# Kernel optimization log

Hardware: AMD Instinct MI355X
Metric: run time of the kernel (lower is better)

## Reference

```python
import jax, jax.numpy as jnp
import numpy as np

D_IN = 768
D_H = 256
N_CTX = 4

def setup_inputs() -> dict:
    key = jax.random.key(0)
    ks = jax.random.split(key, 6)
    b, s = 64, 2048
    return {
        "last_hidden_states": jax.random.normal(ks[0], (b, s, D_IN), dtype=jnp.float32),
        "W1": jax.random.normal(ks[1], (D_IN, D_H), dtype=jnp.float32) / np.sqrt(D_IN),
        "b1": jnp.zeros((D_H,), dtype=jnp.float32),
        "context_vector": jax.random.normal(ks[2], (D_H, N_CTX), dtype=jnp.float32),
        "W2": jax.random.normal(ks[3], (N_CTX * D_IN, D_IN), dtype=jnp.float32) / np.sqrt(N_CTX * D_IN),
        "b2": jnp.zeros((D_IN,), dtype=jnp.float32),
    }

def reference(last_hidden_states, W1, b1, context_vector, W2, b2):
    b = last_hidden_states.shape[0]
    # h: [b, s, 256]
    h = jnp.tanh(jnp.einsum('bsd,dh->bsh', last_hidden_states, W1) + b1)
    # scores over sequence dim for each of 4 context vectors: [b, s, 4]
    scores = jax.nn.softmax(jnp.einsum('bsh,hc->bsc', h, context_vector), axis=1)
    # weighted sums: [b, 4, 768] -> flatten to [b, 3072]
    pooled = jnp.einsum('bsc,bsd->bcd', scores, last_hidden_states).reshape(b, -1)
    pooled = jax.nn.relu(pooled)
    return pooled @ W2 + b2
```

## Files before the change

### kernel.cpp

```cpp
#include <hip/hip_runtime.h>

typedef _Float16 f16x8 __attribute__((ext_vector_type(8)));
typedef float f32x4 __attribute__((ext_vector_type(4)));

#define D_IN 768
#define D_H  256
#define SEQ  2048

__global__ __launch_bounds__(256) void k0_w1t(const float* __restrict__ W1,
                                              _Float16* __restrict__ W1T) {
  __shared__ float tl[64][65];
  const int kb = blockIdx.x, nb = blockIdx.y, t = threadIdx.x;
#pragma unroll
  for (int rep = 0; rep < 16; ++rep) {
    const int row = rep * 4 + (t >> 6), col = t & 63;
    tl[row][col] = W1[(size_t)(kb * 64 + row) * D_H + nb * 64 + col];
  }
  __syncthreads();
#pragma unroll
  for (int rep = 0; rep < 16; ++rep) {
    const int n = rep * 4 + (t >> 6), k = t & 63;
    W1T[(size_t)(nb * 64 + n) * D_IN + kb * 64 + k] = (_Float16)tl[k][n];
  }
}

__global__ __launch_bounds__(512, 2) void kf_fused(const float* __restrict__ X,
    const _Float16* __restrict__ W1T, const float* __restrict__ b1,
    const float* __restrict__ C, _Float16* __restrict__ Ppart,
    float* __restrict__ stats) {
  __shared__ _Float16 Xl[32][776];
  __shared__ float red2[8][32][4];
  __shared__ float red[32][4];
  const int t = threadIdx.x;
  const int bid = blockIdx.x;
  const size_t M0 = (size_t)bid * 32;

  const int xr = t >> 4, xk = (t & 15) * 8;
  const float* Ag = X + (M0 + xr) * D_IN + xk;
  float4 a[12];
#pragma unroll
  for (int s = 0; s < 6; ++s) {
    a[2 * s]     = *(const float4*)(Ag + s * 128);
    a[2 * s + 1] = *(const float4*)(Ag + s * 128 + 4);
  }
#pragma unroll
  for (int s = 0; s < 6; ++s) {
    f16x8 h;
    h[0] = (_Float16)a[2*s].x;   h[1] = (_Float16)a[2*s].y;
    h[2] = (_Float16)a[2*s].z;   h[3] = (_Float16)a[2*s].w;
    h[4] = (_Float16)a[2*s+1].x; h[5] = (_Float16)a[2*s+1].y;
    h[6] = (_Float16)a[2*s+1].z; h[7] = (_Float16)a[2*s+1].w;
    *(f16x8*)&Xl[xr][xk + s * 128] = h;
  }
  __syncthreads();

  const int lane = t & 63, wn = t >> 6;
  const int l15 = lane & 15, kg = lane >> 4;
  const _Float16* Bg0 = W1T + (size_t)(wn * 32 + l15) * D_IN + kg * 8;
  const _Float16* Bg1 = Bg0 + (size_t)16 * D_IN;

  f32x4 acc[2][2];
#pragma unroll
  for (int i = 0; i < 2; ++i)
#pragma unroll
    for (int j = 0; j < 2; ++j) acc[i][j] = f32x4{0.f, 0.f, 0.f, 0.f};

#pragma unroll
  for (int kt = 0; kt < 12; ++kt) {
    f16x8 bf[2][2], af[2][2];
#pragma unroll
    for (int st = 0; st < 2; ++st) {
      bf[0][st] = *(const f16x8*)(Bg0 + kt * 64 + st * 32);
      bf[1][st] = *(const f16x8*)(Bg1 + kt * 64 + st * 32);
      af[0][st] = *(const f16x8*)&Xl[l15][kt * 64 + st * 32 + kg * 8];
      af[1][st] = *(const f16x8*)&Xl[16 + l15][kt * 64 + st * 32 + kg * 8];
    }
#pragma unroll
    for (int st = 0; st < 2; ++st)
#pragma unroll
      for (int j = 0; j < 2; ++j)
#pragma unroll
        for (int i = 0; i < 2; ++i)
          acc[i][j] = __builtin_amdgcn_mfma_f32_16x16x32_f16(af[i][st], bf[j][st], acc[i][j], 0, 0, 0);
  }

  float part[2][4][4];
#pragma unroll
  for (int i = 0; i < 2; ++i)
#pragma unroll
    for (int r = 0; r < 4; ++r)
#pragma unroll
      for (int c = 0; c < 4; ++c) part[i][r][c] = 0.f;

#pragma unroll
  for (int j = 0; j < 2; ++j) {
    const int col = wn * 32 + j * 16 + l15;
    const float4 c4 = *(const float4*)(C + col * 4);
    const float bv = b1[col];
#pragma unroll
    for (int i = 0; i < 2; ++i)
#pragma unroll
      for (int r = 0; r < 4; ++r) {
        float z = acc[i][j][r] + bv;
        z = fminf(fmaxf(z, -15.f), 15.f);
        const float e = __expf(2.f * z);
        const float h = (e - 1.f) / (e + 1.f);
        part[i][r][0] += h * c4.x;
        part[i][r][1] += h * c4.y;
        part[i][r][2] += h * c4.z;
        part[i][r][3] += h * c4.w;
      }
  }
#pragma unroll
  for (int off = 1; off < 16; off <<= 1) {
#pragma unroll
    for (int i = 0; i < 2; ++i)
#pragma unroll
      for (int r = 0; r < 4; ++r)
#pragma unroll
        for (int c = 0; c < 4; ++c)
          part[i][r][c] += __shfl_xor(part[i][r][c], off, 64);
  }
  if (l15 == 0) {
#pragma unroll
    for (int i = 0; i < 2; ++i)
#pragma unroll
      for (int r = 0; r < 4; ++r)
#pragma unroll
        for (int c = 0; c < 4; ++c)
          red2[wn][i * 16 + kg * 4 + r][c] = part[i][r][c];
  }
  __syncthreads();

  if (t < 128) {
    const int r = t >> 2, c = t & 3;
    float v = 0.f;
#pragma unroll
    for (int w = 0; w < 8; ++w) v += red2[w][r][c];
    red[r][c] = v;
  }
  __syncthreads();
  if (t < 256) {
    const int c = t >> 6, r = t & 63;
    const float v = (r < 32) ? red[r][c] : -3.4e38f;
    float m = v;
#pragma unroll
    for (int off = 1; off < 64; off <<= 1) m = fmaxf(m, __shfl_xor(m, off, 64));
    const float e = (r < 32) ? __expf(v - m) : 0.f;
    if (r < 32) red[r][c] = e;
    float s = e;
#pragma unroll
    for (int off = 1; off < 64; off <<= 1) s += __shfl_xor(s, off, 64);
    if (r == 0) {
      stats[(size_t)bid * 8 + c * 2]     = m;
      stats[(size_t)bid * 8 + c * 2 + 1] = s;
    }
  }
  __syncthreads();

  const int pc = t >> 7, pch = t & 127;
  if (pch < 96) {
    float a8[8] = {0.f, 0.f, 0.f, 0.f, 0.f, 0.f, 0.f, 0.f};
#pragma unroll 4
    for (int r = 0; r < 32; ++r) {
      const float w = red[r][pc];
      const f16x8 x8 = *(const f16x8*)&Xl[r][pch * 8];
#pragma unroll
      for (int k = 0; k < 8; ++k) a8[k] += w * (float)x8[k];
    }
    f16x8 o;
#pragma unroll
    for (int k = 0; k < 8; ++k) o[k] = (_Float16)a8[k];
    *(f16x8*)&Ppart[(size_t)bid * 3072 + pc * 768 + pch * 8] = o;
  }
}

__global__ __launch_bounds__(256) void kc_combine(const _Float16* __restrict__ Ppart,
    const float* __restrict__ stats, float* __restrict__ pooled) {
  const int b = blockIdx.x, t = threadIdx.x;
  __shared__ float sm[64][8];
  __shared__ float Mc[4], Dc[4], fw[64][4];
  sm[t >> 2][(t & 3) * 2]     = stats[((size_t)b * 64 + (t >> 2)) * 8 + (t & 3) * 2];
  sm[t >> 2][(t & 3) * 2 + 1] = stats[((size_t)b * 64 + (t >> 2)) * 8 + (t & 3) * 2 + 1];
  __syncthreads();
  if (t < 4) {
    float m = sm[0][t * 2];
#pragma unroll 8
    for (int blk = 1; blk < 64; ++blk) m = fmaxf(m, sm[blk][t * 2]);
    Mc[t] = m;
  }
  __syncthreads();
  {
    const int blk = t >> 2, c = t & 3;
    fw[blk][c] = __expf(sm[blk][c * 2] - Mc[c]);
  }
  __syncthreads();
  if (t < 4) {
    float s = 0.f;
#pragma unroll 8
    for (int blk = 0; blk < 64; ++blk) s += fw[blk][t] * sm[blk][t * 2 + 1];
    Dc[t] = 1.f / s;
  }
  __syncthreads();
#pragma unroll
  for (int c = 0; c < 4; ++c) {
#pragma unroll
    for (int rep = 0; rep < 3; ++rep) {
      const int d = rep * 256 + t;
      float acc = 0.f;
#pragma unroll 8
      for (int blk = 0; blk < 64; ++blk)
        acc += fw[blk][c] * (float)Ppart[((size_t)(b * 64 + blk)) * 3072 + c * 768 + d];
      pooled[(size_t)b * 3072 + c * 768 + d] = fmaxf(acc * Dc[c], 0.f);
    }
  }
}

__global__ __launch_bounds__(256) void k4_partial(const float* __restrict__ pooled,
                                                  const float* __restrict__ W2,
                                                  float* __restrict__ partial) {
  const int jc = blockIdx.x, kc = blockIdx.y, t = threadIdx.x;
  __shared__ float plds[64 * 192];
  __shared__ float sum2[64][64];
  for (int idx = t; idx < 64 * 192; idx += 256) {
    const int b = idx / 192, k = idx - b * 192;
    plds[idx] = pooled[(size_t)b * 3072 + kc * 192 + k];
  }
  __syncthreads();
  const int j = t & 63, kp = t >> 6;
  float acc[64];
#pragma unroll
  for (int b = 0; b < 64; ++b) acc[b] = 0.f;
  const float* W2p = W2 + (size_t)(kc * 192 + kp * 48) * D_IN + jc * 64 + j;
  const float* pb = plds + kp * 48;
  for (int ki = 0; ki < 48; ki += 4) {
    const float w0 = W2p[(size_t)(ki + 0) * D_IN];
    const float w1 = W2p[(size_t)(ki + 1) * D_IN];
    const float w2 = W2p[(size_t)(ki + 2) * D_IN];
    const float w3 = W2p[(size_t)(ki + 3) * D_IN];
#pragma unroll
    for (int b = 0; b < 64; ++b) {
      const float4 p4 = *(const float4*)(pb + b * 192 + ki);
      acc[b] += p4.x * w0 + p4.y * w1 + p4.z * w2 + p4.w * w3;
    }
  }
#pragma unroll
  for (int p = 0; p < 4; ++p) {
    if (kp == p) {
      if (p == 0) {
#pragma unroll
        for (int b = 0; b < 64; ++b) sum2[b][j] = acc[b];
      } else {
#pragma unroll
        for (int b = 0; b < 64; ++b) sum2[b][j] += acc[b];
      }
    }
    __syncthreads();
  }
  for (int idx = t; idx < 4096; idx += 256) {
    const int b = idx >> 6, jj = idx & 63;
    partial[(size_t)kc * 49152 + (size_t)b * D_IN + jc * 64 + jj] = sum2[b][jj];
  }
}

__global__ __launch_bounds__(256) void k5_final(const float* __restrict__ partial,
                                                const float* __restrict__ b2,
                                                float* __restrict__ out) {
  const int o = blockIdx.x * 256 + threadIdx.x;
  float v = b2[o % D_IN];
#pragma unroll
  for (int p = 0; p < 16; ++p) v += partial[(size_t)p * 49152 + o];
  out[o] = v;
}

extern "C" void kernel_launch(void* const* d_in, const int* in_sizes, int n_in,
                              void* d_out, int out_size, void* d_ws, size_t ws_size,
                              hipStream_t stream) {
  const float* X  = (const float*)d_in[0];
  const float* W1 = (const float*)d_in[1];
  const float* b1 = (const float*)d_in[2];
  const float* C  = (const float*)d_in[3];
  const float* W2 = (const float*)d_in[4];
  const float* b2 = (const float*)d_in[5];
  float* out = (float*)d_out;
  char* ws = (char*)d_ws;
  _Float16* W1T   = (_Float16*)ws;
  float* pooled   = (float*)(ws + 393216);
  float* stats    = (float*)(ws + 1179648);
  _Float16* Ppart = (_Float16*)(ws + 1310720);
  float* partial  = (float*)(ws + 1310720);

  k0_w1t    <<<dim3(12, 4), 256, 0, stream>>>(W1, W1T);
  kf_fused  <<<4096,        512, 0, stream>>>(X, W1T, b1, C, Ppart, stats);
  kc_combine<<<64,          256, 0, stream>>>(Ppart, stats, pooled);
  k4_partial<<<dim3(12,16), 256, 0, stream>>>(pooled, W2, partial);
  k5_final  <<<192,         256, 0, stream>>>(partial, b2, out);
}
```

Measured before the change: 324.2 us.

## Restructure fused GEMM to 64-row tiles with async global-to-LDS K-streaming

```diff
diff --git a/kernel.cpp b/kernel.cpp
--- a/kernel.cpp
+++ b/kernel.cpp
@@ -1,11 +1,18 @@
 #include <hip/hip_runtime.h>
 
 typedef _Float16 f16x8 __attribute__((ext_vector_type(8)));
+typedef _Float16 f16x4 __attribute__((ext_vector_type(4)));
 typedef float f32x4 __attribute__((ext_vector_type(4)));
 
 #define D_IN 768
 #define D_H  256
 #define SEQ  2048
+
+__device__ __forceinline__ void gld16(const void* g, void* l) {
+  __builtin_amdgcn_global_load_lds(
+      (const __attribute__((address_space(1))) unsigned int*)g,
+      (__attribute__((address_space(3))) unsigned int*)l, 16, 0, 0);
+}
 
 __global__ __launch_bounds__(256) void k0_w1t(const float* __restrict__ W1,
                                               _Float16* __restrict__ W1T) {
@@ -24,64 +31,83 @@
   }
 }
 
-__global__ __launch_bounds__(512, 2) void kf_fused(const float* __restrict__ X,
+__global__ __launch_bounds__(256, 4) void kf_fused(const float* __restrict__ X,
     const _Float16* __restrict__ W1T, const float* __restrict__ b1,
     const float* __restrict__ C, _Float16* __restrict__ Ppart,
     float* __restrict__ stats) {
-  __shared__ _Float16 Xl[32][776];
-  __shared__ float red2[8][32][4];
-  __shared__ float red[32][4];
+  __shared__ float    Al[64][32];
+  __shared__ _Float16 Bl[256][32];
+  __shared__ float    red2[2][64][4];
+  __shared__ float    red[64][4];
   const int t = threadIdx.x;
   const int bid = blockIdx.x;
-  const size_t M0 = (size_t)bid * 32;
-
-  const int xr = t >> 4, xk = (t & 15) * 8;
-  const float* Ag = X + (M0 + xr) * D_IN + xk;
-  float4 a[12];
-#pragma unroll
-  for (int s = 0; s < 6; ++s) {
-    a[2 * s]     = *(const float4*)(Ag + s * 128);
-    a[2 * s + 1] = *(const float4*)(Ag + s * 128 + 4);
-  }
-#pragma unroll
-  for (int s = 0; s < 6; ++s) {
-    f16x8 h;
-    h[0] = (_Float16)a[2*s].x;   h[1] = (_Float16)a[2*s].y;
-    h[2] = (_Float16)a[2*s].z;   h[3] = (_Float16)a[2*s].w;
-    h[4] = (_Float16)a[2*s+1].x; h[5] = (_Float16)a[2*s+1].y;
-    h[6] = (_Float16)a[2*s+1].z; h[7] = (_Float16)a[2*s+1].w;
-    *(f16x8*)&Xl[xr][xk + s * 128] = h;
-  }
-  __syncthreads();
-
-  const int lane = t & 63, wn = t >> 6;
-  const int l15 = lane & 15, kg = lane >> 4;
-  const _Float16* Bg0 = W1T + (size_t)(wn * 32 + l15) * D_IN + kg * 8;
-  const _Float16* Bg1 = Bg0 + (size_t)16 * D_IN;
-
-  f32x4 acc[2][2];
+  const size_t M0 = (size_t)bid * 64;
+
+  const int l = t & 63, w = t >> 6;
+  const int ar0 = (w * 2 + 0) * 8 + (l >> 3);
+  const int ar1 = (w * 2 + 1) * 8 + (l >> 3);
+  const int aj = l & 7;
+  const float* As0 = X + (M0 + ar0) * D_IN + ((aj ^ (ar0 & 7)) * 4);
+  const float* As1 = X + (M0 + ar1) * D_IN + ((aj ^ (ar1 & 7)) * 4);
+  char* Ad0 = (char*)Al + (w * 2 + 0) * 1024 + l * 16;
+  char* Ad1 = (char*)Al + (w * 2 + 1) * 1024 + l * 16;
+  const int bj = l & 3;
+  const int bc0 = (w * 4 + 0) * 16 + (l >> 2);
+  const int bc1 = (w * 4 + 1) * 16 + (l >> 2);
+  const int bc2 = (w * 4 + 2) * 16 + (l >> 2);
+  const int bc3 = (w * 4 + 3) * 16 + (l >> 2);
+  const _Float16* Bs0 = W1T + (size_t)bc0 * D_IN + ((bj ^ (bc0 & 3)) * 8);
+  const _Float16* Bs1 = W1T + (size_t)bc1 * D_IN + ((bj ^ (bc1 & 3)) * 8);
+  const _Float16* Bs2 = W1T + (size_t)bc2 * D_IN + ((bj ^ (bc2 & 3)) * 8);
+  const _Float16* Bs3 = W1T + (size_t)bc3 * D_IN + ((bj ^ (bc3 & 3)) * 8);
+  char* Bd0 = (char*)Bl + (w * 4 + 0) * 1024 + l * 16;
+  char* Bd1 = (char*)Bl + (w * 4 + 1) * 1024 + l * 16;
+  char* Bd2 = (char*)Bl + (w * 4 + 2) * 1024 + l * 16;
+  char* Bd3 = (char*)Bl + (w * 4 + 3) * 1024 + l * 16;
+
+  const int wm = w >> 1, wn = w & 1;
+  const int l15 = l & 15, kg = l >> 4;
+  const int r0 = wm * 32 + l15, r1 = r0 + 16;
+  const int sA0lo = ((2 * kg) ^ (r0 & 7)) * 4, sA0hi = ((2 * kg + 1) ^ (r0 & 7)) * 4;
+  const int sA1lo = ((2 * kg) ^ (r1 & 7)) * 4, sA1hi = ((2 * kg + 1) ^ (r1 & 7)) * 4;
+
+  f32x4 acc[2][8];
 #pragma unroll
   for (int i = 0; i < 2; ++i)
 #pragma unroll
-    for (int j = 0; j < 2; ++j) acc[i][j] = f32x4{0.f, 0.f, 0.f, 0.f};
-
-#pragma unroll
-  for (int kt = 0; kt < 12; ++kt) {
-    f16x8 bf[2][2], af[2][2];
-#pragma unroll
-    for (int st = 0; st < 2; ++st) {
-      bf[0][st] = *(const f16x8*)(Bg0 + kt * 64 + st * 32);
-      bf[1][st] = *(const f16x8*)(Bg1 + kt * 64 + st * 32);
-      af[0][st] = *(const f16x8*)&Xl[l15][kt * 64 + st * 32 + kg * 8];
-      af[1][st] = *(const f16x8*)&Xl[16 + l15][kt * 64 + st * 32 + kg * 8];
-    }
-#pragma unroll
-    for (int st = 0; st < 2; ++st)
-#pragma unroll
-      for (int j = 0; j < 2; ++j)
-#pragma unroll
-        for (int i = 0; i < 2; ++i)
-          acc[i][j] = __builtin_amdgcn_mfma_f32_16x16x32_f16(af[i][st], bf[j][st], acc[i][j], 0, 0, 0);
+    for (int n = 0; n < 8; ++n) acc[i][n] = f32x4{0.f, 0.f, 0.f, 0.f};
+
+  for (int kt = 0; kt < 24; ++kt) {
+    const int ko = kt * 32;
+    gld16(As0 + ko, Ad0);
+    gld16(As1 + ko, Ad1);
+    gld16(Bs0 + ko, Bd0);
+    gld16(Bs1 + ko, Bd1);
+    gld16(Bs2 + ko, Bd2);
+    gld16(Bs3 + ko, Bd3);
+    __syncthreads();
+
+    const float4 a0lo = *(const float4*)&Al[r0][sA0lo];
+    const float4 a0hi = *(const float4*)&Al[r0][sA0hi];
+    const float4 a1lo = *(const float4*)&Al[r1][sA1lo];
+    const float4 a1hi = *(const float4*)&Al[r1][sA1hi];
+    f16x8 af0, af1;
+    af0[0] = (_Float16)a0lo.x; af0[1] = (_Float16)a0lo.y;
+    af0[2] = (_Float16)a0lo.z; af0[3] = (_Float16)a0lo.w;
+    af0[4] = (_Float16)a0hi.x; af0[5] = (_Float16)a0hi.y;
+    af0[6] = (_Float16)a0hi.z; af0[7] = (_Float16)a0hi.w;
+    af1[0] = (_Float16)a1lo.x; af1[1] = (_Float16)a1lo.y;
+    af1[2] = (_Float16)a1lo.z; af1[3] = (_Float16)a1lo.w;
+    af1[4] = (_Float16)a1hi.x; af1[5] = (_Float16)a1hi.y;
+    af1[6] = (_Float16)a1hi.z; af1[7] = (_Float16)a1hi.w;
+#pragma unroll
+    for (int n = 0; n < 8; ++n) {
+      const int col = wn * 128 + n * 16 + l15;
+      const f16x8 bf = *(const f16x8*)&Bl[col][(kg ^ (col & 3)) * 8];
+      acc[0][n] = __builtin_amdgcn_mfma_f32_16x16x32_f16(af0, bf, acc[0][n], 0, 0, 0);
+      acc[1][n] = __builtin_amdgcn_mfma_f32_16x16x32_f16(af1, bf, acc[1][n], 0, 0, 0);
+    }
+    __syncthreads();
   }
 
   float part[2][4][4];
@@ -93,15 +119,15 @@
       for (int c = 0; c < 4; ++c) part[i][r][c] = 0.f;
 
 #pragma unroll
-  for (int j = 0; j < 2; ++j) {
-    const int col = wn * 32 + j * 16 + l15;
+  for (int n = 0; n < 8; ++n) {
+    const int col = wn * 128 + n * 16 + l15;
     const float4 c4 = *(const float4*)(C + col * 4);
     const float bv = b1[col];
 #pragma unroll
     for (int i = 0; i < 2; ++i)
 #pragma unroll
       for (int r = 0; r < 4; ++r) {
-        float z = acc[i][j][r] + bv;
+        float z = acc[i][n][r] + bv;
         z = fminf(fmaxf(z, -15.f), 15.f);
         const float e = __expf(2.f * z);
         const float h = (e - 1.f) / (e + 1.f);
@@ -128,26 +154,23 @@
       for (int r = 0; r < 4; ++r)
 #pragma unroll
         for (int c = 0; c < 4; ++c)
-          red2[wn][i * 16 + kg * 4 + r][c] = part[i][r][c];
-  }
-  __syncthreads();
-
-  if (t < 128) {
+          red2[wn][wm * 32 + i * 16 + kg * 4 + r][c] = part[i][r][c];
+  }
+  __syncthreads();
+
+  {
     const int r = t >> 2, c = t & 3;
-    float v = 0.f;
-#pragma unroll
-    for (int w = 0; w < 8; ++w) v += red2[w][r][c];
-    red[r][c] = v;
-  }
-  __syncthreads();
-  if (t < 256) {
+    red[r][c] = red2[0][r][c] + red2[1][r][c];
+  }
+  __syncthreads();
+  {
     const int c = t >> 6, r = t & 63;
-    const float v = (r < 32) ? red[r][c] : -3.4e38f;
+    const float v = red[r][c];
     float m = v;
 #pragma unroll
     for (int off = 1; off < 64; off <<= 1) m = fmaxf(m, __shfl_xor(m, off, 64));
-    const float e = (r < 32) ? __expf(v - m) : 0.f;
-    if (r < 32) red[r][c] = e;
+    const float e = __expf(v - m);
+    red[r][c] = e;
     float s = e;
 #pragma unroll
     for (int off = 1; off < 64; off <<= 1) s += __shfl_xor(s, off, 64);
@@ -158,47 +181,57 @@
   }
   __syncthreads();
 
-  const int pc = t >> 7, pch = t & 127;
-  if (pch < 96) {
-    float a8[8] = {0.f, 0.f, 0.f, 0.f, 0.f, 0.f, 0.f, 0.f};
+  if (t < 192) {
+    float pacc[4][4];
+#pragma unroll
+    for (int c = 0; c < 4; ++c)
+#pragma unroll
+      for (int j = 0; j < 4; ++j) pacc[c][j] = 0.f;
+    const float* Xp = X + M0 * D_IN + t * 4;
 #pragma unroll 4
-    for (int r = 0; r < 32; ++r) {
-      const float w = red[r][pc];
-      const f16x8 x8 = *(const f16x8*)&Xl[r][pch * 8];
-#pragma unroll
-      for (int k = 0; k < 8; ++k) a8[k] += w * (float)x8[k];
-    }
-    f16x8 o;
-#pragma unroll
-    for (int k = 0; k < 8; ++k) o[k] = (_Float16)a8[k];
-    *(f16x8*)&Ppart[(size_t)bid * 3072 + pc * 768 + pch * 8] = o;
+    for (int r = 0; r < 64; ++r) {
+      const float4 x4 = *(const float4*)(Xp + (size_t)r * D_IN);
+      const float4 w4 = *(const float4*)&red[r][0];
+      const float wc[4] = {w4.x, w4.y, w4.z, w4.w};
+      const float xv[4] = {x4.x, x4.y, x4.z, x4.w};
+#pragma unroll
+      for (int c = 0; c < 4; ++c)
+#pragma unroll
+        for (int j = 0; j < 4; ++j) pacc[c][j] += wc[c] * xv[j];
+    }
+#pragma unroll
+    for (int c = 0; c < 4; ++c) {
+      f16x4 o;
+#pragma unroll
+      for (int j = 0; j < 4; ++j) o[j] = (_Float16)pacc[c][j];
+      *(f16x4*)&Ppart[(size_t)bid * 3072 + c * 768 + t * 4] = o;
+    }
   }
 }
 
 __global__ __launch_bounds__(256) void kc_combine(const _Float16* __restrict__ Ppart,
     const float* __restrict__ stats, float* __restrict__ pooled) {
   const int b = blockIdx.x, t = threadIdx.x;
-  __shared__ float sm[64][8];
-  __shared__ float Mc[4], Dc[4], fw[64][4];
-  sm[t >> 2][(t & 3) * 2]     = stats[((size_t)b * 64 + (t >> 2)) * 8 + (t & 3) * 2];
-  sm[t >> 2][(t & 3) * 2 + 1] = stats[((size_t)b * 64 + (t >> 2)) * 8 + (t & 3) * 2 + 1];
+  __shared__ float sm[32][8];
+  __shared__ float Mc[4], Dc[4], fw[32][4];
+  sm[t >> 3][t & 7] = stats[((size_t)b * 32 + (t >> 3)) * 8 + (t & 7)];
   __syncthreads();
   if (t < 4) {
     float m = sm[0][t * 2];
-#pragma unroll 8
-    for (int blk = 1; blk < 64; ++blk) m = fmaxf(m, sm[blk][t * 2]);
+#pragma unroll
+    for (int blk = 1; blk < 32; ++blk) m = fmaxf(m, sm[blk][t * 2]);
     Mc[t] = m;
   }
   __syncthreads();
-  {
+  if (t < 128) {
     const int blk = t >> 2, c = t & 3;
     fw[blk][c] = __expf(sm[blk][c * 2] - Mc[c]);
   }
   __syncthreads();
   if (t < 4) {
     float s = 0.f;
-#pragma unroll 8
-    for (int blk = 0; blk < 64; ++blk) s += fw[blk][t] * sm[blk][t * 2 + 1];
+#pragma unroll
+    for (int blk = 0; blk < 32; ++blk) s += fw[blk][t] * sm[blk][t * 2 + 1];
     Dc[t] = 1.f / s;
   }
   __syncthreads();
@@ -208,9 +241,9 @@
     for (int rep = 0; rep < 3; ++rep) {
       const int d = rep * 256 + t;
       float acc = 0.f;
-#pragma unroll 8
-      for (int blk = 0; blk < 64; ++blk)
-        acc += fw[blk][c] * (float)Ppart[((size_t)(b * 64 + blk)) * 3072 + c * 768 + d];
+#pragma unroll 4
+      for (int blk = 0; blk < 32; ++blk)
+        acc += fw[blk][c] * (float)Ppart[((size_t)(b * 32 + blk)) * 3072 + c * 768 + d];
       pooled[(size_t)b * 3072 + c * 768 + d] = fmaxf(acc * Dc[c], 0.f);
     }
   }
@@ -287,11 +320,11 @@
   _Float16* W1T   = (_Float16*)ws;
   float* pooled   = (float*)(ws + 393216);
   float* stats    = (float*)(ws + 1179648);
-  _Float16* Ppart = (_Float16*)(ws + 1310720);
-  float* partial  = (float*)(ws + 1310720);
+  _Float16* Ppart = (_Float16*)(ws + 1245184);
+  float* partial  = (float*)(ws + 1245184);
 
   k0_w1t    <<<dim3(12, 4), 256, 0, stream>>>(W1, W1T);
-  kf_fused  <<<4096,        512, 0, stream>>>(X, W1T, b1, C, Ppart, stats);
+  kf_fused  <<<2048,        256, 0, stream>>>(X, W1T, b1, C, Ppart, stats);
   kc_combine<<<64,          256, 0, stream>>>(Ppart, stats, pooled);
   k4_partial<<<dim3(12,16), 256, 0, stream>>>(pooled, W2, partial);
   k5_final  <<<192,         256, 0, stream>>>(partial, b2, out);
```

Measured after the change: 307.5 us. 5.1% less time.

## Shrink fused block to 256 threads with wider per-wave N tile

Applied to the files above, without the earlier changes.

```diff
diff --git a/kernel.cpp b/kernel.cpp
--- a/kernel.cpp
+++ b/kernel.cpp
@@ -1,6 +1,7 @@
 #include <hip/hip_runtime.h>
 
 typedef _Float16 f16x8 __attribute__((ext_vector_type(8)));
+typedef _Float16 f16x4 __attribute__((ext_vector_type(4)));
 typedef float f32x4 __attribute__((ext_vector_type(4)));
 
 #define D_IN 768
@@ -24,64 +25,67 @@
   }
 }
 
-__global__ __launch_bounds__(512, 2) void kf_fused(const float* __restrict__ X,
+__global__ __launch_bounds__(256, 3) void kf_fused(const float* __restrict__ X,
     const _Float16* __restrict__ W1T, const float* __restrict__ b1,
     const float* __restrict__ C, _Float16* __restrict__ Ppart,
     float* __restrict__ stats) {
   __shared__ _Float16 Xl[32][776];
-  __shared__ float red2[8][32][4];
+  __shared__ float red2[4][32][4];
   __shared__ float red[32][4];
   const int t = threadIdx.x;
   const int bid = blockIdx.x;
   const size_t M0 = (size_t)bid * 32;
 
-  const int xr = t >> 4, xk = (t & 15) * 8;
-  const float* Ag = X + (M0 + xr) * D_IN + xk;
-  float4 a[12];
-#pragma unroll
-  for (int s = 0; s < 6; ++s) {
-    a[2 * s]     = *(const float4*)(Ag + s * 128);
-    a[2 * s + 1] = *(const float4*)(Ag + s * 128 + 4);
-  }
-#pragma unroll
-  for (int s = 0; s < 6; ++s) {
-    f16x8 h;
-    h[0] = (_Float16)a[2*s].x;   h[1] = (_Float16)a[2*s].y;
-    h[2] = (_Float16)a[2*s].z;   h[3] = (_Float16)a[2*s].w;
-    h[4] = (_Float16)a[2*s+1].x; h[5] = (_Float16)a[2*s+1].y;
-    h[6] = (_Float16)a[2*s+1].z; h[7] = (_Float16)a[2*s+1].w;
-    *(f16x8*)&Xl[xr][xk + s * 128] = h;
-  }
-  __syncthreads();
-
-  const int lane = t & 63, wn = t >> 6;
-  const int l15 = lane & 15, kg = lane >> 4;
-  const _Float16* Bg0 = W1T + (size_t)(wn * 32 + l15) * D_IN + kg * 8;
-  const _Float16* Bg1 = Bg0 + (size_t)16 * D_IN;
-
-  f32x4 acc[2][2];
+  const float* Xbase = X + M0 * D_IN;
+  float4 L0[12], L1[12];
+#pragma unroll
+  for (int i = 0; i < 12; ++i)
+    L0[i] = *(const float4*)(Xbase + (size_t)(i * 256 + t) * 4);
+#pragma unroll
+  for (int i = 0; i < 12; ++i)
+    L1[i] = *(const float4*)(Xbase + (size_t)((12 + i) * 256 + t) * 4);
+#pragma unroll
+  for (int i = 0; i < 12; ++i) {
+    const int f = i * 256 + t;
+    const int row = f / 192;
+    const int jj = f - row * 192;
+    f16x4 h;
+    h[0] = (_Float16)L0[i].x; h[1] = (_Float16)L0[i].y;
+    h[2] = (_Float16)L0[i].z; h[3] = (_Float16)L0[i].w;
+    *(f16x4*)&Xl[row][jj * 4] = h;
+  }
+#pragma unroll
+  for (int i = 0; i < 12; ++i) {
+    const int f = (12 + i) * 256 + t;
+    const int row = f / 192;
+    const int jj = f - row * 192;
+    f16x4 h;
+    h[0] = (_Float16)L1[i].x; h[1] = (_Float16)L1[i].y;
+    h[2] = (_Float16)L1[i].z; h[3] = (_Float16)L1[i].w;
+    *(f16x4*)&Xl[row][jj * 4] = h;
+  }
+  __syncthreads();
+
+  const int l = t & 63, wn = t >> 6;
+  const int l15 = l & 15, kg = l >> 4;
+
+  f32x4 acc[2][4];
 #pragma unroll
   for (int i = 0; i < 2; ++i)
 #pragma unroll
-    for (int j = 0; j < 2; ++j) acc[i][j] = f32x4{0.f, 0.f, 0.f, 0.f};
-
-#pragma unroll
-  for (int kt = 0; kt < 12; ++kt) {
-    f16x8 bf[2][2], af[2][2];
-#pragma unroll
-    for (int st = 0; st < 2; ++st) {
-      bf[0][st] = *(const f16x8*)(Bg0 + kt * 64 + st * 32);
-      bf[1][st] = *(const f16x8*)(Bg1 + kt * 64 + st * 32);
-      af[0][st] = *(const f16x8*)&Xl[l15][kt * 64 + st * 32 + kg * 8];
-      af[1][st] = *(const f16x8*)&Xl[16 + l15][kt * 64 + st * 32 + kg * 8];
-    }
-#pragma unroll
-    for (int st = 0; st < 2; ++st)
-#pragma unroll
-      for (int j = 0; j < 2; ++j)
-#pragma unroll
-        for (int i = 0; i < 2; ++i)
-          acc[i][j] = __builtin_amdgcn_mfma_f32_16x16x32_f16(af[i][st], bf[j][st], acc[i][j], 0, 0, 0);
+    for (int g = 0; g < 4; ++g) acc[i][g] = f32x4{0.f, 0.f, 0.f, 0.f};
+
+#pragma unroll
+  for (int kt = 0; kt < 24; ++kt) {
+    const f16x8 af0 = *(const f16x8*)&Xl[l15][kt * 32 + kg * 8];
+    const f16x8 af1 = *(const f16x8*)&Xl[16 + l15][kt * 32 + kg * 8];
+#pragma unroll
+    for (int g = 0; g < 4; ++g) {
+      const int col = wn * 64 + g * 16 + l15;
+      const f16x8 bf = *(const f16x8*)(W1T + (size_t)col * D_IN + kt * 32 + kg * 8);
+      acc[0][g] = __builtin_amdgcn_mfma_f32_16x16x32_f16(af0, bf, acc[0][g], 0, 0, 0);
+      acc[1][g] = __builtin_amdgcn_mfma_f32_16x16x32_f16(af1, bf, acc[1][g], 0, 0, 0);
+    }
   }
 
   float part[2][4][4];
@@ -93,15 +97,15 @@
       for (int c = 0; c < 4; ++c) part[i][r][c] = 0.f;
 
 #pragma unroll
-  for (int j = 0; j < 2; ++j) {
-    const int col = wn * 32 + j * 16 + l15;
+  for (int g = 0; g < 4; ++g) {
+    const int col = wn * 64 + g * 16 + l15;
     const float4 c4 = *(const float4*)(C + col * 4);
     const float bv = b1[col];
 #pragma unroll
     for (int i = 0; i < 2; ++i)
 #pragma unroll
       for (int r = 0; r < 4; ++r) {
-        float z = acc[i][j][r] + bv;
+        float z = acc[i][g][r] + bv;
         z = fminf(fmaxf(z, -15.f), 15.f);
         const float e = __expf(2.f * z);
         const float h = (e - 1.f) / (e + 1.f);
@@ -134,13 +138,10 @@
 
   if (t < 128) {
     const int r = t >> 2, c = t & 3;
-    float v = 0.f;
-#pragma unroll
-    for (int w = 0; w < 8; ++w) v += red2[w][r][c];
-    red[r][c] = v;
-  }
-  __syncthreads();
-  if (t < 256) {
+    red[r][c] = red2[0][r][c] + red2[1][r][c] + red2[2][r][c] + red2[3][r][c];
+  }
+  __syncthreads();
+  {
     const int c = t >> 6, r = t & 63;
     const float v = (r < 32) ? red[r][c] : -3.4e38f;
     float m = v;
@@ -158,20 +159,22 @@
   }
   __syncthreads();
 
-  const int pc = t >> 7, pch = t & 127;
-  if (pch < 96) {
-    float a8[8] = {0.f, 0.f, 0.f, 0.f, 0.f, 0.f, 0.f, 0.f};
-#pragma unroll 4
-    for (int r = 0; r < 32; ++r) {
-      const float w = red[r][pc];
-      const f16x8 x8 = *(const f16x8*)&Xl[r][pch * 8];
-#pragma unroll
-      for (int k = 0; k < 8; ++k) a8[k] += w * (float)x8[k];
-    }
-    f16x8 o;
-#pragma unroll
-    for (int k = 0; k < 8; ++k) o[k] = (_Float16)a8[k];
-    *(f16x8*)&Ppart[(size_t)bid * 3072 + pc * 768 + pch * 8] = o;
+  {
+    const int c = t >> 6;
+    for (int g = (t & 63); g < 96; g += 64) {
+      float a8[8] = {0.f, 0.f, 0.f, 0.f, 0.f, 0.f, 0.f, 0.f};
+#pragma unroll 8
+      for (int r = 0; r < 32; ++r) {
+        const float w = red[r][c];
+        const f16x8 x8 = *(const f16x8*)&Xl[r][g * 8];
+#pragma unroll
+        for (int k = 0; k < 8; ++k) a8[k] += w * (float)x8[k];
+      }
+      f16x8 o;
+#pragma unroll
+      for (int k = 0; k < 8; ++k) o[k] = (_Float16)a8[k];
+      *(f16x8*)&Ppart[(size_t)bid * 3072 + c * 768 + g * 8] = o;
+    }
   }
 }
 
@@ -291,7 +294,7 @@
   float* partial  = (float*)(ws + 1310720);
 
   k0_w1t    <<<dim3(12, 4), 256, 0, stream>>>(W1, W1T);
-  kf_fused  <<<4096,        512, 0, stream>>>(X, W1T, b1, C, Ppart, stats);
+  kf_fused  <<<4096,        256, 0, stream>>>(X, W1T, b1, C, Ppart, stats);
   kc_combine<<<64,          256, 0, stream>>>(Ppart, stats, pooled);
   k4_partial<<<dim3(12,16), 256, 0, stream>>>(pooled, W2, partial);
   k5_final  <<<192,         256, 0, stream>>>(partial, b2, out);
```

After: 349.5 us. +7.8%, slower.
